# Kernel optimization log

Hardware: AMD Instinct MI355X
Metric: run time of the kernel (lower is better)

Reference implementation:

```python
import jax, jax.numpy as jnp
import numpy as np

NUM_PERTS = 20000
D = 256          # embedding_dim
B, C = 64, 512   # batch_size, num_cells
EPS = 1e-5


def setup_inputs() -> dict:
    key = jax.random.key(0)
    ks = jax.random.split(key, 20)
    inp = {
        'perturbation_ids': jax.random.randint(ks[0], (B, C), 0, NUM_PERTS),
        'table': jax.random.normal(ks[1], (NUM_PERTS, D), dtype=jnp.float32),
    }
    s = 1.0 / np.sqrt(D)
    for i in range(4):
        inp[f'W{i+1}'] = jax.random.uniform(ks[2 + 2 * i], (D, D), minval=-s, maxval=s, dtype=jnp.float32)
        inp[f'b{i+1}'] = jax.random.uniform(ks[3 + 2 * i], (D,), minval=-s, maxval=s, dtype=jnp.float32)
    for i in range(3):
        inp[f'g{i+1}'] = jnp.ones((D,), jnp.float32)
        inp[f'be{i+1}'] = jnp.zeros((D,), jnp.float32)
    return inp


def _bn(x, gamma, beta):
    # BatchNorm1d forward with batch statistics (training-mode math, biased var)
    mu = jnp.mean(x, axis=0)
    var = jnp.mean(jnp.square(x - mu), axis=0)
    return (x - mu) * jax.lax.rsqrt(var + EPS) * gamma + beta


def reference(perturbation_ids, table,
              W1, b1, W2, b2, W3, b3, W4, b4,
              g1, be1, g2, be2, g3, be3):
    # Vectorized replacement of the Python double-loop dict gather
    emb = table[perturbation_ids]                 # (B, C, D)
    x = emb.reshape(-1, D)                        # (B*C, D)
    x = _bn(jax.nn.gelu(x @ W1 + b1, approximate=False), g1, be1)
    x = _bn(jax.nn.gelu(x @ W2 + b2, approximate=False), g2, be2)
    x = _bn(jax.nn.gelu(x @ W3 + b3, approximate=False), g3, be3)
    x = jax.nn.gelu(x @ W4 + b4, approximate=False)
    return x.reshape(B, C, D)
```

## Files before the change

### kernel.cpp

```cpp
#include <hip/hip_runtime.h>
#include <math.h>


typedef __attribute__((ext_vector_type(8))) short short8;
typedef __attribute__((ext_vector_type(4))) float floatx4;

#define DDIM 256
#define NBLK 512

struct Params {
    const int* ids;
    const float* table;
    const float* b[4];
    const float* g[3];
    const float* be[3];
    const unsigned short* Wt;
    float* stats;
    unsigned int* barrier;
    float* out;
};

__device__ __forceinline__ unsigned short f2bf(float f) {
    union { float f; unsigned int u; } v; v.f = f;
    unsigned int r = v.u + 0x7fffu + ((v.u >> 16) & 1u);
    return (unsigned short)(r >> 16);
}
__device__ __forceinline__ float bf2f(unsigned short u) {
    union { unsigned int i; float f; } v; v.i = ((unsigned int)u) << 16;
    return v.f;
}
__device__ __forceinline__ float gelu_fast(float x) {
    float z = 0.7978845608f * (x + 0.044715f * x * x * x);
    float e = __expf(2.0f * z);
    float th = 1.0f - 2.0f * __builtin_amdgcn_rcpf(1.0f + e);
    return 0.5f * x * (1.0f + th);
}

__global__ void prep_kernel(const float* __restrict__ W0,
                            const float* __restrict__ W1,
                            const float* __restrict__ W2,
                            const float* __restrict__ W3,
                            unsigned short* __restrict__ Wt,
                            float* __restrict__ stats,
                            unsigned int* __restrict__ barrier)
{
    const int t = threadIdx.x, b = blockIdx.x;
    const int j = b >> 8, n = b & 255;
    const float* W = (j == 0) ? W0 : (j == 1) ? W1 : (j == 2) ? W2 : W3;
    Wt[((size_t)j << 16) + (size_t)n * DDIM + t] = f2bf(W[(size_t)t * DDIM + n]);
    if (b < 12) {
        float* s = stats + b * 1024;
        s[t] = 0.f; s[t + 256] = 0.f; s[t + 512] = 0.f; s[t + 768] = 0.f;
    }
    if (b == 12) { barrier[t] = 0u; barrier[t + 256] = 0u; }
}

__device__ __forceinline__ void grid_barrier(unsigned int* base, int phase)
{
    unsigned int* cnt  = base + phase * 16;
    unsigned int* flag = base + 256 + phase * 16;
    __syncthreads();
    if (threadIdx.x == 0) {
        asm volatile("s_waitcnt vmcnt(0)" ::: "memory");
        unsigned int old = __hip_atomic_fetch_add(cnt, 1u, __ATOMIC_RELAXED,
                                                  __HIP_MEMORY_SCOPE_AGENT);
        if (old == (unsigned)(NBLK - 1)) {
            __hip_atomic_store(flag, 1u, __ATOMIC_RELAXED,
                               __HIP_MEMORY_SCOPE_AGENT);
        } else {
            int cap = 2000000;
            while (!__hip_atomic_load(flag, __ATOMIC_RELAXED,
                                      __HIP_MEMORY_SCOPE_AGENT)) {
                __builtin_amdgcn_s_sleep(8);
                if (--cap == 0) break;
            }
        }
    }
    __syncthreads();
}

template<int GATHER, int AFFINE, int LAST>
__device__ __forceinline__ void layer_step(
    unsigned short* P, float* sc, float* sh,
    const Params& p,
    const unsigned short* Wt, const float* bias,
    const float* statsIn, const float* gma, const float* bta,
    float* statShards)
{
    const int tid  = threadIdx.x;
    const int blk  = blockIdx.x;
    const int wave = tid >> 6;
    const int lane = tid & 63;
    const int quad = lane >> 4;
    const int l15  = lane & 15;
    const int row0 = blk * 64;

    if (AFFINE) {
        if (tid < 256) {
            float sum = 0.f, sq = 0.f;
#pragma unroll
            for (int s = 0; s < 8; ++s) {
                sum += __hip_atomic_load(&statsIn[s * 512 + tid],
                                         __ATOMIC_RELAXED, __HIP_MEMORY_SCOPE_AGENT);
                sq  += __hip_atomic_load(&statsIn[s * 512 + 256 + tid],
                                         __ATOMIC_RELAXED, __HIP_MEMORY_SCOPE_AGENT);
            }
            const float mu  = sum * (1.f / 32768.f);
            const float var = sq * (1.f / 32768.f) - mu * mu;
            const float scl = rsqrtf(var + 1e-5f) * gma[tid];
            sc[tid] = scl;
            sh[tid] = bta[tid] - mu * scl;
        }
        __syncthreads();
    }

    {
        const int r     = tid >> 3;
        const int gbase = (tid & 7) * 4;
        if (GATHER) {
            const int src = p.ids[row0 + r];
            const float* tp = p.table + (size_t)src * DDIM + gbase * 8;
#pragma unroll
            for (int j = 0; j < 4; ++j) {
                float4 v0 = *(const float4*)(tp + j * 8);
                float4 v1 = *(const float4*)(tp + j * 8 + 4);
                union { unsigned short u[8]; uint4 v; } o;
                o.u[0]=f2bf(v0.x); o.u[1]=f2bf(v0.y); o.u[2]=f2bf(v0.z); o.u[3]=f2bf(v0.w);
                o.u[4]=f2bf(v1.x); o.u[5]=f2bf(v1.y); o.u[6]=f2bf(v1.z); o.u[7]=f2bf(v1.w);
                const int g = gbase + j;
                *(uint4*)(P + r * 256 + ((g ^ (r & 7)) << 3)) = o.v;
            }
        } else {
#pragma unroll
            for (int j = 0; j < 4; ++j) {
                const int g = gbase + j;
                unsigned short* slot = P + r * 256 + ((g ^ (r & 7)) << 3);
                union { unsigned short u[8]; uint4 v; } o;
                o.v = *(const uint4*)slot;
#pragma unroll
                for (int e = 0; e < 8; ++e) {
                    const int c = g * 8 + e;
                    o.u[e] = f2bf(fmaf(bf2f(o.u[e]), sc[c], sh[c]));
                }
                *(uint4*)slot = o.v;
            }
        }
    }

    float bias_v[2];
#pragma unroll
    for (int nt = 0; nt < 2; ++nt)
        bias_v[nt] = bias[wave * 32 + nt * 16 + l15];

    floatx4 acc[4][2];
#pragma unroll
    for (int i = 0; i < 4; ++i)
#pragma unroll
        for (int j = 0; j < 2; ++j)
            acc[i][j] = floatx4{0.f, 0.f, 0.f, 0.f};

    __syncthreads();

    const unsigned short* wb = Wt + (size_t)(wave * 32 + l15) * DDIM + quad * 8;
    short8 bfr[2], bnx[2], af[4], anx[4];
    {
        const int agp = (quad ^ (l15 & 7)) * 8;
#pragma unroll
        for (int nt = 0; nt < 2; ++nt)
            bfr[nt] = *(const short8*)(wb + (size_t)(nt * 16) * DDIM);
#pragma unroll
        for (int mt = 0; mt < 4; ++mt)
            af[mt] = *(const short8*)(P + (mt * 16 + l15) * 256 + agp);
    }
#pragma unroll
    for (int kk = 0; kk < 8; ++kk) {
        if (kk < 7) {
            const int agp = (((kk + 1) * 4 + quad) ^ (l15 & 7)) * 8;
#pragma unroll
            for (int nt = 0; nt < 2; ++nt)
                bnx[nt] = *(const short8*)(wb + (size_t)(nt * 16) * DDIM
                                           + (kk + 1) * 32);
#pragma unroll
            for (int mt = 0; mt < 4; ++mt)
                anx[mt] = *(const short8*)(P + (mt * 16 + l15) * 256 + agp);
        }
#pragma unroll
        for (int mt = 0; mt < 4; ++mt)
#pragma unroll
            for (int nt = 0; nt < 2; ++nt)
                acc[mt][nt] = __builtin_amdgcn_mfma_f32_16x16x32_bf16(
                    af[mt], bfr[nt], acc[mt][nt], 0, 0, 0);
#pragma unroll
        for (int x = 0; x < 4; ++x) af[x] = anx[x];
#pragma unroll
        for (int x = 0; x < 2; ++x) bfr[x] = bnx[x];
    }

    if (!LAST) __syncthreads();

    float s1[2] = {0.f, 0.f};
    float s2[2] = {0.f, 0.f};
#pragma unroll
    for (int mt = 0; mt < 4; ++mt) {
#pragma unroll
        for (int nt = 0; nt < 2; ++nt) {
            const int col = wave * 32 + nt * 16 + l15;
#pragma unroll
            for (int i = 0; i < 4; ++i) {
                const int r = mt * 16 + quad * 4 + i;
                float y = gelu_fast(acc[mt][nt][i] + bias_v[nt]);
                if (LAST) {
                    p.out[(size_t)(row0 + r) * DDIM + col] = y;
                } else {
                    const int g = col >> 3;
                    P[r * 256 + ((g ^ (r & 7)) << 3) + (col & 7)] = f2bf(y);
                    s1[nt] += y; s2[nt] += y * y;
                }
            }
        }
    }
    if (!LAST) {
#pragma unroll
        for (int nt = 0; nt < 2; ++nt) {
            s1[nt] += __shfl_xor(s1[nt], 16); s1[nt] += __shfl_xor(s1[nt], 32);
            s2[nt] += __shfl_xor(s2[nt], 16); s2[nt] += __shfl_xor(s2[nt], 32);
        }
        float* sb = statShards + (blk & 7) * 512;
        if (quad == 0) {
#pragma unroll
            for (int nt = 0; nt < 2; ++nt) {
                const int col = wave * 32 + nt * 16 + l15;
                atomicAdd(&sb[col],       s1[nt]);
                atomicAdd(&sb[256 + col], s2[nt]);
            }
        }
    }
}

__global__ __launch_bounds__(512, 4) void fused_enc(Params p)
{
    __shared__ alignas(16) unsigned short P[64 * 256];
    __shared__ float sc[256], sh[256];

    layer_step<1, 0, 0>(P, sc, sh, p, p.Wt,          p.b[0],
                        nullptr,         nullptr, nullptr, p.stats);
    grid_barrier(p.barrier, 0);
    layer_step<0, 1, 0>(P, sc, sh, p, p.Wt + 65536,  p.b[1],
                        p.stats,         p.g[0],  p.be[0], p.stats + 4096);
    grid_barrier(p.barrier, 1);
    layer_step<0, 1, 0>(P, sc, sh, p, p.Wt + 131072, p.b[2],
                        p.stats + 4096,  p.g[1],  p.be[1], p.stats + 8192);
    grid_barrier(p.barrier, 2);
    layer_step<0, 1, 1>(P, sc, sh, p, p.Wt + 196608, p.b[3],
                        p.stats + 8192,  p.g[2],  p.be[2], nullptr);
}

extern "C" void kernel_launch(void* const* d_in, const int* in_sizes, int n_in,
                              void* d_out, int out_size, void* d_ws, size_t ws_size,
                              hipStream_t stream)
{
    const float* W1 = (const float*)d_in[2];
    const float* W2 = (const float*)d_in[4];
    const float* W3 = (const float*)d_in[6];
    const float* W4 = (const float*)d_in[8];

    Params pp;
    pp.ids   = (const int*)  d_in[0];
    pp.table = (const float*)d_in[1];
    pp.b[0] = (const float*)d_in[3];
    pp.b[1] = (const float*)d_in[5];
    pp.b[2] = (const float*)d_in[7];
    pp.b[3] = (const float*)d_in[9];
    pp.g[0] = (const float*)d_in[10]; pp.be[0] = (const float*)d_in[11];
    pp.g[1] = (const float*)d_in[12]; pp.be[1] = (const float*)d_in[13];
    pp.g[2] = (const float*)d_in[14]; pp.be[2] = (const float*)d_in[15];

    unsigned char* ws = (unsigned char*)d_ws;
    unsigned short* Wt = (unsigned short*)ws;
    float* stats       = (float*)(ws + (size_t)524288);
    unsigned int* bar  = (unsigned int*)(ws + (size_t)589824);

    pp.Wt      = Wt;
    pp.stats   = stats;
    pp.barrier = bar;
    pp.out     = (float*)d_out;

    prep_kernel<<<1024, 256, 0, stream>>>(W1, W2, W3, W4, Wt, stats, bar);
    fused_enc<<<dim3(NBLK), dim3(512), 0, stream>>>(pp);
}
```

Measured before the change: 175.1 us.

## Tile weight transpose through LDS and use two-level hierarchical grid barrier

The weight prep kernel now transposes 64x64 tiles through shared memory with float4 reads and 16-byte writes, running 64 blocks instead of 1024 and giving coalesced access in both directions. The grid barrier becomes two-level: blocks first increment one of 8 group counters (64 blocks each), and the last arriver of each group increments a root counter, which spreads atomic contention across several addresses. Barrier state now uses 256 words per phase, so the zeroed region grows to 1024 words. Risks are extra atomic latency on the critical path and dependence on the enlarged barrier layout fitting in the workspace.

```diff
diff --git a/kernel.cpp b/kernel.cpp
--- a/kernel.cpp
+++ b/kernel.cpp
@@ -36,38 +36,67 @@
     return 0.5f * x * (1.0f + th);
 }
 
-__global__ void prep_kernel(const float* __restrict__ W0,
-                            const float* __restrict__ W1,
-                            const float* __restrict__ W2,
-                            const float* __restrict__ W3,
-                            unsigned short* __restrict__ Wt,
-                            float* __restrict__ stats,
-                            unsigned int* __restrict__ barrier)
-{
+__global__ __launch_bounds__(256) void prep_kernel(
+    const float* __restrict__ W0, const float* __restrict__ W1,
+    const float* __restrict__ W2, const float* __restrict__ W3,
+    unsigned short* __restrict__ Wt, float* __restrict__ stats,
+    unsigned int* __restrict__ barrier)
+{
+    __shared__ unsigned short T[64][68];
     const int t = threadIdx.x, b = blockIdx.x;
-    const int j = b >> 8, n = b & 255;
+    const int j  = b >> 4;
+    const int kr = ((b >> 2) & 3) * 64;
+    const int nc = (b & 3) * 64;
     const float* W = (j == 0) ? W0 : (j == 1) ? W1 : (j == 2) ? W2 : W3;
-    Wt[((size_t)j << 16) + (size_t)n * DDIM + t] = f2bf(W[(size_t)t * DDIM + n]);
-    if (b < 12) {
-        float* s = stats + b * 1024;
-        s[t] = 0.f; s[t + 256] = 0.f; s[t + 512] = 0.f; s[t + 768] = 0.f;
-    }
-    if (b == 12) { barrier[t] = 0u; barrier[t + 256] = 0u; }
+
+    {
+        const int k = t >> 2, c0 = (t & 3) * 16;
+        const float* src = W + (size_t)(kr + k) * DDIM + nc + c0;
+#pragma unroll
+        for (int i = 0; i < 4; ++i) {
+            float4 v = *(const float4*)(src + i * 4);
+            T[k][c0 + i * 4 + 0] = f2bf(v.x);
+            T[k][c0 + i * 4 + 1] = f2bf(v.y);
+            T[k][c0 + i * 4 + 2] = f2bf(v.z);
+            T[k][c0 + i * 4 + 3] = f2bf(v.w);
+        }
+    }
+    __syncthreads();
+    {
+        const int n = t >> 2, kc = (t & 3) * 16;
+        union { unsigned short u[16]; uint4 v[2]; } o;
+#pragma unroll
+        for (int i = 0; i < 16; ++i) o.u[i] = T[kc + i][n];
+        uint4* dst = (uint4*)(Wt + ((size_t)j << 16)
+                              + (size_t)(nc + n) * DDIM + kr + kc);
+        dst[0] = o.v[0]; dst[1] = o.v[1];
+    }
+    if (b < 48)       stats[b * 256 + t] = 0.f;
+    else if (b < 52)  barrier[(b - 48) * 256 + t] = 0u;
 }
 
 __device__ __forceinline__ void grid_barrier(unsigned int* base, int phase)
 {
-    unsigned int* cnt  = base + phase * 16;
-    unsigned int* flag = base + 256 + phase * 16;
+    unsigned int* ph = base + phase * 256;
     __syncthreads();
     if (threadIdx.x == 0) {
         asm volatile("s_waitcnt vmcnt(0)" ::: "memory");
-        unsigned int old = __hip_atomic_fetch_add(cnt, 1u, __ATOMIC_RELAXED,
+        unsigned int* gc   = ph + (blockIdx.x >> 6) * 16;
+        unsigned int* root = ph + 128;
+        unsigned int* flag = ph + 192;
+        bool done = false;
+        unsigned int old = __hip_atomic_fetch_add(gc, 1u, __ATOMIC_RELAXED,
                                                   __HIP_MEMORY_SCOPE_AGENT);
-        if (old == (unsigned)(NBLK - 1)) {
-            __hip_atomic_store(flag, 1u, __ATOMIC_RELAXED,
-                               __HIP_MEMORY_SCOPE_AGENT);
-        } else {
+        if (old == 63u) {
+            unsigned int r = __hip_atomic_fetch_add(root, 1u, __ATOMIC_RELAXED,
+                                                    __HIP_MEMORY_SCOPE_AGENT);
+            if (r == 7u) {
+                __hip_atomic_store(flag, 1u, __ATOMIC_RELAXED,
+                                   __HIP_MEMORY_SCOPE_AGENT);
+                done = true;
+            }
+        }
+        if (!done) {
             int cap = 2000000;
             while (!__hip_atomic_load(flag, __ATOMIC_RELAXED,
                                       __HIP_MEMORY_SCOPE_AGENT)) {
@@ -285,6 +314,6 @@
     pp.barrier = bar;
     pp.out     = (float*)d_out;
 
-    prep_kernel<<<1024, 256, 0, stream>>>(W1, W2, W3, W4, Wt, stats, bar);
+    prep_kernel<<<64, 256, 0, stream>>>(W1, W2, W3, W4, Wt, stats, bar);
     fused_enc<<<dim3(NBLK), dim3(512), 0, stream>>>(pp);
 }
```

Result: faster. 167.4 us (-4.4%).
